# Optimization experiments

Measured on AMD Instinct MI355X. Metric: run time of the kernel, lower is better.

Reference implementation:

```python
import jax, jax.numpy as jnp
import numpy as np

LATENT = 128
K = 1024          # num_embeddings
LENGTH = 128
HID = 200         # LSTM hidden
IN = 768
COND = 1536


def setup_inputs() -> dict:
    key = jax.random.key(0)
    ks = jax.random.split(key, 16)
    B = 256
    x = jax.random.normal(ks[0], (B, 1, LENGTH, IN), dtype=jnp.float32)
    condition = jax.random.normal(ks[1], (B, 1, LENGTH, COND), dtype=jnp.float32)
    noise = jax.random.normal(ks[2], (B, IN), dtype=jnp.float32)
    s = 0.05
    # LSTM params (PyTorch gate order: i, f, g, o)
    W_ih = jax.random.normal(ks[3], (4 * HID, IN), dtype=jnp.float32) * s
    W_hh = jax.random.normal(ks[4], (4 * HID, HID), dtype=jnp.float32) * s
    b_ih = jax.random.normal(ks[5], (4 * HID,), dtype=jnp.float32) * s
    b_hh = jax.random.normal(ks[6], (4 * HID,), dtype=jnp.float32) * s
    # encoder fc: HID -> LATENT
    W_enc = jax.random.normal(ks[7], (LATENT, HID), dtype=jnp.float32) * s
    b_enc = jnp.zeros((LATENT,), dtype=jnp.float32)
    # codebook, uniform(-1/K, 1/K) as in the module
    emb = jax.random.uniform(ks[8], (K, LATENT), minval=-1.0 / K, maxval=1.0 / K, dtype=jnp.float32)
    # decoder MLP
    D1_IN = LATENT + COND + IN  # 2432
    W1 = jax.random.normal(ks[9], (200, D1_IN), dtype=jnp.float32) * s
    b1 = jnp.zeros((200,), dtype=jnp.float32)
    W2 = jax.random.normal(ks[10], (400, 200), dtype=jnp.float32) * s
    b2 = jnp.zeros((400,), dtype=jnp.float32)
    W3 = jax.random.normal(ks[11], (IN, 400), dtype=jnp.float32) * s
    b3 = jnp.zeros((IN,), dtype=jnp.float32)
    return {"x": x, "condition": condition, "noise": noise,
            "W_ih": W_ih, "W_hh": W_hh, "b_ih": b_ih, "b_hh": b_hh,
            "W_enc": W_enc, "b_enc": b_enc, "emb": emb,
            "W1": W1, "b1": b1, "W2": W2, "b2": b2, "W3": W3, "b3": b3}


def _lstm_last_h(xs, W_ih, W_hh, b_ih, b_hh):
    # xs: [B, T, IN] -> final hidden state [B, HID]
    B = xs.shape[0]
    h0 = jnp.zeros((B, HID), dtype=xs.dtype)
    c0 = jnp.zeros((B, HID), dtype=xs.dtype)
    # precompute input projections for all timesteps: [T, B, 4H]
    gates_x = jnp.einsum('bti,gi->tbg', xs, W_ih) + b_ih + b_hh

    def step(carry, gx):
        h, c = carry
        g = gx + h @ W_hh.T  # [B, 4H]
        i, f, gg, o = jnp.split(g, 4, axis=-1)
        c = jax.nn.sigmoid(f) * c + jax.nn.sigmoid(i) * jnp.tanh(gg)
        h = jax.nn.sigmoid(o) * jnp.tanh(c)
        return (h, c), None

    (h, _), _ = jax.lax.scan(step, (h0, c0), gates_x)
    return h


def reference(x, condition, noise, W_ih, W_hh, b_ih, b_hh, W_enc, b_enc, emb,
              W1, b1, W2, b2, W3, b3):
    B = x.shape[0]
    # Encoder
    xs = x.reshape(B, -1, IN)                      # [B, T, 768]
    h = _lstm_last_h(xs, W_ih, W_hh, b_ih, b_hh)   # [B, 200]
    z_e = h @ W_enc.T + b_enc                      # [B, latent]
    # VectorQuantizer: squared-distance argmin + gather
    d = (jnp.sum(z_e * z_e, axis=-1, keepdims=True)
         + jnp.sum(emb * emb, axis=1)
         - 2.0 * z_e @ emb.T)                      # [B, K]
    indices = jnp.argmin(d, axis=-1)               # [B]
    z_q = emb[indices]                             # [B, latent]
    # Decoder (forward uses z_q directly)
    L = LENGTH
    z = jnp.broadcast_to(z_q[:, None, None, :], (B, 1, L, LATENT))
    n = jnp.broadcast_to(noise[:, None, None, :], (B, 1, L, IN))
    zc = jnp.concatenate([z, condition, n], axis=-1)  # [B,1,L,2432]
    h1 = jax.nn.relu(zc @ W1.T + b1)
    h2 = jax.nn.relu(h1 @ W2.T + b2)
    out = jax.nn.sigmoid(h2 @ W3.T + b3)
    return out.reshape(-1, 1, L, IN)
```

## Files before the change

kernel.cpp:

```cpp
#include <hip/hip_runtime.h>
#include <math.h>

typedef unsigned short u16;
typedef u16 u16x8 __attribute__((ext_vector_type(8)));
typedef __bf16 bf16x8 __attribute__((ext_vector_type(8)));
typedef float f32x4 __attribute__((ext_vector_type(4)));

#define HID 200
#define G4H 800
#define TLEN 128
#define LATENT 128
#define NCODES 1024
#define DIN 768
#define DCOND 1536
#define NB 256
#define MROWS (NB * TLEN)
#define LDG 896
#define LDH1 256
#define LDH2 512
#define NOUT 768

#define WSCL 400.0f
#define HSCL 127.0f
#define ISCL (1.0f / (WSCL * HSCL))
#define W4_DWORDS (12 * 800 * 4)
#define W4_BYTES (W4_DWORDS * 4)

__device__ __forceinline__ u16 f2b(float f) {
  union { float f; unsigned u; } v; v.f = f;
  unsigned r = v.u + 0x7fffu + ((v.u >> 16) & 1u);
  return (u16)(r >> 16);
}
__device__ __forceinline__ float b2f(u16 h) {
  union { unsigned u; float f; } v; v.u = ((unsigned)h) << 16;
  return v.f;
}
__device__ __forceinline__ float sigf(float x) { return 1.f / (1.f + __expf(-x)); }
__device__ __forceinline__ float tanh_fast(float x) {
  return 1.f - 2.f / (__expf(2.f * x) + 1.f);
}

__device__ __forceinline__ int dot4(unsigned a, unsigned b, int c) {
#if __has_builtin(__builtin_amdgcn_sdot4)
  return __builtin_amdgcn_sdot4((int)a, (int)b, c, false);
#else
  int s = c;
  s += (int)(signed char)(a) * (int)(signed char)(b);
  s += (int)(signed char)(a >> 8) * (int)(signed char)(b >> 8);
  s += (int)(signed char)(a >> 16) * (int)(signed char)(b >> 16);
  s += (int)(signed char)(a >> 24) * (int)(signed char)(b >> 24);
  return s;
#endif
}

__device__ __forceinline__ void gl16(const void* g, void* l) {
  __builtin_amdgcn_global_load_lds(
      (const __attribute__((address_space(1))) void*)g,
      (__attribute__((address_space(3))) void*)l, 16, 0, 0);
}

__device__ __forceinline__ unsigned cvtpk(float a, float b) {
  unsigned r;
  asm("v_cvt_pk_bf16_f32 %0, %1, %2" : "=v"(r) : "v"(a), "v"(b));
  return r;
}

__global__ void cvt_pad(const float* __restrict__ src, u16* __restrict__ dst,
                        int nr, int nc, int lds, int col0, int NRp, int KP) {
  int i = blockIdx.x * blockDim.x + threadIdx.x;
  if (i >= NRp * KP) return;
  int r = i / KP, c = i - r * KP;
  float v = (r < nr && c < nc) ? src[(size_t)r * lds + col0 + c] : 0.f;
  dst[i] = f2b(v);
}

__global__ void pad_f32(const float* __restrict__ src, float* __restrict__ dst,
                        int n, int npad) {
  int i = blockIdx.x * blockDim.x + threadIdx.x;
  if (i < npad) dst[i] = (i < n) ? src[i] : 0.f;
}

__global__ void pack_whh_i8(const float* __restrict__ Whh, unsigned* __restrict__ W4,
                            unsigned* __restrict__ Wreg,
                            const float* __restrict__ b_ih, const float* __restrict__ b_hh,
                            float* __restrict__ biasc) {
  int i = blockIdx.x * blockDim.x + threadIdx.x;
  if (i < 800 * 50) {
    int row = i / 50, dw = i - row * 50;
    unsigned d = 0;
#pragma unroll
    for (int e = 0; e < 4; ++e) {
      int k = dw * 4 + e;
      float w = Whh[(size_t)row * HID + k] * WSCL;
      int q = (int)lrintf(w);
      q = q > 127 ? 127 : (q < -127 ? -127 : q);
      d |= ((unsigned)(q & 0xFF)) << (8 * e);
    }
    if (dw < 48) {
      W4[(dw >> 2) * 3200 + row * 4 + (dw & 3)] = d;
    } else {
      int r = (row < 400) ? row : row - 400;
      int base = (row < 400) ? 0 : 2;
      Wreg[r * 4 + base + (dw - 48)] = d;
    }
  }
  if (i < LDG) biasc[i] = (i < G4H) ? (b_ih[i] + b_hh[i]) : 0.f;
}

enum { EPI_GATES = 0, EPI_H1 = 1, EPI_H2 = 2, EPI_OUT = 3 };

__device__ __forceinline__ f32x4 mfma16(bf16x8 a, bf16x8 b, f32x4 c) {
  return __builtin_amdgcn_mfma_f32_16x16x32_bf16(a, b, c, 0, 0, 0);
}

template<bool AF32, int EPI>
__global__ __launch_bounds__(256) void gemm_bf16(
    const void* __restrict__ Ap, const u16* __restrict__ Bp,
    void* __restrict__ Cp, int K, int ldc, const float* __restrict__ bias) {
  __shared__ __attribute__((aligned(16))) char AsRaw[AF32 ? 128 * 32 * 4 : 128 * 32 * 2];
  __shared__ __attribute__((aligned(16))) u16 Bs[128 * 32];
  float* Asf = (float*)AsRaw;
  u16* As16 = (u16*)AsRaw;

  const int t = threadIdx.x;
  const int tileN = blockIdx.x * 128;
  const int tileM = blockIdx.y * 128;
  const int l = t & 63;
  const int w = t >> 6;
  const int wr = (w >> 1) * 64;
  const int wc = (w & 1) * 64;
  const int fr = l & 15;
  const int fg = l >> 4;

  const u16* bsrc[2];
  u16* bdst[2];
#pragma unroll
  for (int j = 0; j < 2; ++j) {
    int tb = w * 1024 + j * 4096 + (t & 63) * 16;
    int row = tb >> 6, gd = (tb >> 4) & 3;
    bsrc[j] = Bp + (size_t)(tileN + row) * K + ((gd ^ ((row >> 1) & 3)) << 3);
    bdst[j] = Bs + w * 512 + j * 2048;
  }
  const float* asrcF[4];
  float* adstF[4];
  const u16* asrcH[2];
  u16* adstH[2];
  if constexpr (AF32) {
#pragma unroll
    for (int j = 0; j < 4; ++j) {
      int tb = w * 1024 + j * 4096 + (t & 63) * 16;
      int row = tb >> 7, gd = (tb >> 4) & 7;
      asrcF[j] = (const float*)Ap + (size_t)(tileM + row) * K + ((gd ^ (row & 7)) << 2);
      adstF[j] = Asf + w * 256 + j * 1024;
    }
  } else {
#pragma unroll
    for (int j = 0; j < 2; ++j) {
      int tb = w * 1024 + j * 4096 + (t & 63) * 16;
      int row = tb >> 6, gd = (tb >> 4) & 3;
      asrcH[j] = (const u16*)Ap + (size_t)(tileM + row) * K + ((gd ^ ((row >> 1) & 3)) << 3);
      adstH[j] = As16 + w * 512 + j * 2048;
    }
  }

  f32x4 acc[4][4];
#pragma unroll
  for (int m = 0; m < 4; ++m)
#pragma unroll
    for (int n = 0; n < 4; ++n) {
      f32x4 z = {0.f, 0.f, 0.f, 0.f};
      acc[m][n] = z;
    }

  for (int k0 = 0; k0 < K; k0 += 32) {
#pragma unroll
    for (int j = 0; j < 2; ++j) { gl16(bsrc[j], bdst[j]); bsrc[j] += 32; }
    if constexpr (AF32) {
#pragma unroll
      for (int j = 0; j < 4; ++j) { gl16(asrcF[j], adstF[j]); asrcF[j] += 32; }
    } else {
#pragma unroll
      for (int j = 0; j < 2; ++j) { gl16(asrcH[j], adstH[j]); asrcH[j] += 32; }
    }
    __syncthreads();

    bf16x8 av[4], bv[4];
#pragma unroll
    for (int m = 0; m < 4; ++m) {
      const int row = wr + m * 16 + fr;
      if constexpr (AF32) {
        const int g0 = (2 * fg) ^ (row & 7);
        const int g1 = (2 * fg + 1) ^ (row & 7);
        float4 p0 = *(const float4*)(Asf + row * 32 + g0 * 4);
        float4 p1 = *(const float4*)(Asf + row * 32 + g1 * 4);
        uint4 u;
        u.x = cvtpk(p0.x, p0.y); u.y = cvtpk(p0.z, p0.w);
        u.z = cvtpk(p1.x, p1.y); u.w = cvtpk(p1.z, p1.w);
        av[m] = __builtin_bit_cast(bf16x8, u);
      } else {
        const int g = fg ^ ((row >> 1) & 3);
        av[m] = __builtin_bit_cast(bf16x8, *(const u16x8*)(As16 + row * 32 + g * 8));
      }
    }
#pragma unroll
    for (int n = 0; n < 4; ++n) {
      const int row = wc + n * 16 + fr;
      const int g = fg ^ ((row >> 1) & 3);
      bv[n] = __builtin_bit_cast(bf16x8, *(const u16x8*)(Bs + row * 32 + g * 8));
    }
#pragma unroll
    for (int m = 0; m < 4; ++m)
#pragma unroll
      for (int n = 0; n < 4; ++n)
        acc[m][n] = mfma16(av[m], bv[n], acc[m][n]);
    __syncthreads();
  }

#pragma unroll
  for (int m = 0; m < 4; ++m) {
#pragma unroll
    for (int n = 0; n < 4; ++n) {
      const int gcol = tileN + wc + n * 16 + fr;
      const int growb = tileM + wr + m * 16 + fg * 4;
#pragma unroll
      for (int r = 0; r < 4; ++r) {
        const int grow = growb + r;
        float v = acc[m][n][r];
        if constexpr (EPI == EPI_GATES) {
          v += bias[gcol];
          ((u16*)Cp)[(size_t)grow * ldc + gcol] = f2b(v);
        } else if constexpr (EPI == EPI_H1) {
          v += bias[(grow >> 7) * 256 + gcol];
          v = fmaxf(v, 0.f);
          ((u16*)Cp)[(size_t)grow * ldc + gcol] = f2b(v);
        } else if constexpr (EPI == EPI_H2) {
          v += bias[gcol];
          v = fmaxf(v, 0.f);
          ((u16*)Cp)[(size_t)grow * ldc + gcol] = f2b(v);
        } else {
          v += bias[gcol];
          ((float*)Cp)[(size_t)grow * ldc + gcol] = sigf(v);
        }
      }
    }
  }
}

__global__ __launch_bounds__(448) void lstm_enc(
    const u16* __restrict__ gates, const uint4* __restrict__ W4g,
    const uint4* __restrict__ Wregg,
    const float* __restrict__ Wenc, const float* __restrict__ b_enc,
    const float* __restrict__ emb, const float* __restrict__ W1,
    const float* __restrict__ b1, const float* __restrict__ noise,
    float* __restrict__ p1) {
  extern __shared__ __attribute__((aligned(16))) char dynsm[];
  uint4* W4 = (uint4*)dynsm;
  __shared__ __attribute__((aligned(16))) unsigned sh_hq[56];
  __shared__ __attribute__((aligned(16))) float sh_hf[HID];
  __shared__ float sh_g[G4H];
  __shared__ __attribute__((aligned(16))) float sh_ze[LATENT];
  __shared__ float sh_zq[LATENT];
  __shared__ float sh_rd[448];
  __shared__ int sh_ri[448];
  const int r = threadIdx.x;
  const int b = blockIdx.x;
  const bool active = (r < 400);

  for (int i = r; i < 12 * 800; i += 448) W4[i] = W4g[i];
  uint4 wreg = active ? Wregg[r] : (uint4){0, 0, 0, 0};
  if (r < 56) sh_hq[r] = 0;
  if (r < HID) sh_hf[r] = 0.f;
  float c = 0.f;
  const u16* gp = gates + (size_t)b * TLEN * LDG + r;
  float gvA = 0.f, gvB = 0.f;
  if (active) { gvA = b2f(gp[0]); gvB = b2f(gp[400]); }
  __syncthreads();

  for (int t = 0; t < TLEN; ++t) {
    gp += LDG;
    float gvA_n = 0.f, gvB_n = 0.f;
    if (active && t + 1 < TLEN) { gvA_n = b2f(gp[0]); gvB_n = b2f(gp[400]); }

    if (active) {
      unsigned hd[52];
#pragma unroll
      for (int j = 0; j < 13; ++j) {
        uint4 v = ((const uint4*)sh_hq)[j];
        hd[4 * j + 0] = v.x; hd[4 * j + 1] = v.y;
        hd[4 * j + 2] = v.z; hd[4 * j + 3] = v.w;
      }
      int accA = 0, accB = 0;
#pragma unroll
      for (int jb = 0; jb < 12; ++jb) {
        uint4 wA = W4[jb * 800 + r];
        uint4 wB = W4[jb * 800 + 400 + r];
        accA = dot4(wA.x, hd[4 * jb + 0], accA);
        accA = dot4(wA.y, hd[4 * jb + 1], accA);
        accA = dot4(wA.z, hd[4 * jb + 2], accA);
        accA = dot4(wA.w, hd[4 * jb + 3], accA);
        accB = dot4(wB.x, hd[4 * jb + 0], accB);
        accB = dot4(wB.y, hd[4 * jb + 1], accB);
        accB = dot4(wB.z, hd[4 * jb + 2], accB);
        accB = dot4(wB.w, hd[4 * jb + 3], accB);
      }
      accA = dot4(wreg.x, hd[48], accA);
      accA = dot4(wreg.y, hd[49], accA);
      accB = dot4(wreg.z, hd[48], accB);
      accB = dot4(wreg.w, hd[49], accB);
      sh_g[r] = gvA + (float)accA * ISCL;
      sh_g[r + 400] = gvB + (float)accB * ISCL;
    }
    __syncthreads();
    if (r < HID) {
      float gi = sh_g[r], gf = sh_g[HID + r], gg = sh_g[2 * HID + r], go = sh_g[3 * HID + r];
      c = sigf(gf) * c + sigf(gi) * tanh_fast(gg);
      float h = sigf(go) * tanh_fast(c);
      sh_hf[r] = h;
      int q = __float2int_rn(h * HSCL);
      ((char*)sh_hq)[r] = (char)q;
    }
    __syncthreads();
    gvA = gvA_n; gvB = gvB_n;
  }

  if (r < LATENT) {
    float z = b_enc[r];
#pragma unroll 4
    for (int k = 0; k < HID; ++k) z = fmaf(Wenc[(size_t)r * HID + k], sh_hf[k], z);
    sh_ze[r] = z;
  }
  __syncthreads();

  float best = INFINITY; int bi = 0;
  for (int k = r; k < NCODES; k += 448) {
    float d = 0.f;
#pragma unroll
    for (int q = 0; q < LATENT / 4; ++q) {
      float4 e = *(const float4*)&emb[(size_t)k * LATENT + q * 4];
      float4 z = *(const float4*)&sh_ze[q * 4];
      d += e.x * (e.x - 2.f * z.x) + e.y * (e.y - 2.f * z.y)
         + e.z * (e.z - 2.f * z.z) + e.w * (e.w - 2.f * z.w);
    }
    if (d < best) { best = d; bi = k; }
  }
  sh_rd[r] = best; sh_ri[r] = bi;
  __syncthreads();
  for (int s = 256; s > 0; s >>= 1) {
    if (r < s && r + s < 448) {
      float od = sh_rd[r + s]; int oi = sh_ri[r + s];
      if (od < sh_rd[r] || (od == sh_rd[r] && oi < sh_ri[r])) { sh_rd[r] = od; sh_ri[r] = oi; }
    }
    __syncthreads();
  }
  const int kmin = sh_ri[0];
  if (r < LATENT) sh_zq[r] = emb[(size_t)kmin * LATENT + r];
  __syncthreads();

  if (r < 256) {
    float v = 0.f;
    if (r < HID) {
      v = b1[r];
      const float* wrow = W1 + (size_t)r * 2432;
#pragma unroll 4
      for (int d = 0; d < LATENT; ++d) v = fmaf(wrow[d], sh_zq[d], v);
      const float* nz = noise + (size_t)b * DIN;
#pragma unroll 4
      for (int d = 0; d < DIN; ++d) v = fmaf(wrow[1664 + d], nz[d], v);
    }
    p1[b * 256 + r] = v;
  }
}

extern "C" void kernel_launch(void* const* d_in, const int* in_sizes, int n_in,
                              void* d_out, int out_size, void* d_ws, size_t ws_size,
                              hipStream_t stream) {
  const float* x     = (const float*)d_in[0];
  const float* cond  = (const float*)d_in[1];
  const float* noise = (const float*)d_in[2];
  const float* W_ih  = (const float*)d_in[3];
  const float* W_hh  = (const float*)d_in[4];
  const float* b_ih  = (const float*)d_in[5];
  const float* b_hh  = (const float*)d_in[6];
  const float* W_enc = (const float*)d_in[7];
  const float* b_enc = (const float*)d_in[8];
  const float* emb   = (const float*)d_in[9];
  const float* W1    = (const float*)d_in[10];
  const float* b1    = (const float*)d_in[11];
  const float* W2    = (const float*)d_in[12];
  const float* b2    = (const float*)d_in[13];
  const float* W3    = (const float*)d_in[14];
  const float* b3    = (const float*)d_in[15];

  char* ws = (char*)d_ws;
  size_t off = 0;
  auto alloc = [&](size_t bytes) -> void* {
    void* p = ws + off; off += (bytes + 255) & ~(size_t)255; return p;
  };
  u16*      W_ihb = (u16*)alloc((size_t)896 * 768 * 2);
  u16*      W1cb  = (u16*)alloc((size_t)256 * 1536 * 2);
  u16*      W2b   = (u16*)alloc((size_t)512 * 256 * 2);
  u16*      W3b   = (u16*)alloc((size_t)768 * 512 * 2);
  float*    b2p   = (float*)alloc(512 * 4);
  unsigned* W4    = (unsigned*)alloc((size_t)W4_BYTES);
  unsigned* Wreg  = (unsigned*)alloc((size_t)400 * 4 * 4);
  float*    biasc = (float*)alloc(LDG * 4);
  u16*      gates = (u16*)alloc((size_t)MROWS * LDG * 2);
  float*    p1    = (float*)alloc(256 * 256 * 4);
  u16*      h1    = (u16*)alloc((size_t)MROWS * LDH1 * 2);
  u16*      h2    = (u16*)alloc((size_t)MROWS * LDH2 * 2);

  cvt_pad<<<dim3((896 * 768 + 255) / 256), 256, 0, stream>>>(W_ih, W_ihb, 800, 768, 768, 0, 896, 768);
  cvt_pad<<<dim3((256 * 1536 + 255) / 256), 256, 0, stream>>>(W1, W1cb, 200, 1536, 2432, 128, 256, 1536);
  cvt_pad<<<dim3((512 * 256 + 255) / 256), 256, 0, stream>>>(W2, W2b, 400, 200, 200, 0, 512, 256);
  cvt_pad<<<dim3((768 * 512 + 255) / 256), 256, 0, stream>>>(W3, W3b, 768, 400, 400, 0, 768, 512);
  pad_f32<<<dim3(2), 256, 0, stream>>>(b2, b2p, 400, 512);
  pack_whh_i8<<<dim3((800 * 50 + 255) / 256), 256, 0, stream>>>(W_hh, W4, Wreg, b_ih, b_hh, biasc);

  gemm_bf16<true, EPI_GATES><<<dim3(LDG / 128, MROWS / 128), 256, 0, stream>>>(
      x, W_ihb, gates, 768, LDG, biasc);

  static bool attr_set = false;
  if (!attr_set) {
    (void)hipFuncSetAttribute((const void*)lstm_enc,
                              hipFuncAttributeMaxDynamicSharedMemorySize, W4_BYTES);
    attr_set = true;
  }
  lstm_enc<<<dim3(NB), 448, W4_BYTES, stream>>>(gates, (const uint4*)W4, (const uint4*)Wreg,
                                                W_enc, b_enc, emb, W1, b1, noise, p1);

  gemm_bf16<true, EPI_H1><<<dim3(LDH1 / 128, MROWS / 128), 256, 0, stream>>>(
      cond, W1cb, h1, DCOND, LDH1, p1);
  gemm_bf16<false, EPI_H2><<<dim3(LDH2 / 128, MROWS / 128), 256, 0, stream>>>(
      h1, W2b, h2, LDH1, LDH2, b2p);
  gemm_bf16<false, EPI_OUT><<<dim3(NOUT / 128, MROWS / 128), 256, 0, stream>>>(
      h2, W3b, (float*)d_out, LDH2, NOUT, b3);
}
```

Before: 552.6 us.

## Compute all four LSTM gates per hidden unit in-thread, double-buffer h

The LSTM step is restructured so each of 200 threads computes all four gate dot products for one hidden unit and applies the cell update directly. This removes the shared-memory gate exchange and halves the barriers per timestep by double-buffering the quantized hidden state. The block shrinks from 448 to 256 threads, and the tail-weight layout is repacked to match. Each thread now does twice the dot-product work per step with fewer threads in flight, so per-step latency could grow.

```diff
diff --git a/kernel.cpp b/kernel.cpp
--- a/kernel.cpp
+++ b/kernel.cpp
@@ -23,8 +23,8 @@
 #define WSCL 400.0f
 #define HSCL 127.0f
 #define ISCL (1.0f / (WSCL * HSCL))
-#define W4_DWORDS (12 * 800 * 4)
-#define W4_BYTES (W4_DWORDS * 4)
+#define W4_UINT4 (12 * 800)
+#define W4_BYTES (W4_UINT4 * 16)
 
 __device__ __forceinline__ u16 f2b(float f) {
   union { float f; unsigned u; } v; v.f = f;
@@ -97,11 +97,10 @@
       d |= ((unsigned)(q & 0xFF)) << (8 * e);
     }
     if (dw < 48) {
-      W4[(dw >> 2) * 3200 + row * 4 + (dw & 3)] = d;
+      W4[((dw >> 2) * 800 + row) * 4 + (dw & 3)] = d;
     } else {
-      int r = (row < 400) ? row : row - 400;
-      int base = (row < 400) ? 0 : 2;
-      Wreg[r * 4 + base + (dw - 48)] = d;
+      int g = row / 200, u = row - g * 200;
+      Wreg[u * 8 + g * 2 + (dw - 48)] = d;
     }
   }
   if (i < LDG) biasc[i] = (i < G4H) ? (b_ih[i] + b_hh[i]) : 0.f;
@@ -246,82 +245,89 @@
   }
 }
 
-__global__ __launch_bounds__(448) void lstm_enc(
+__global__ __launch_bounds__(256) void lstm_enc(
     const u16* __restrict__ gates, const uint4* __restrict__ W4g,
-    const uint4* __restrict__ Wregg,
+    const uint4* __restrict__ WregG,
     const float* __restrict__ Wenc, const float* __restrict__ b_enc,
     const float* __restrict__ emb, const float* __restrict__ W1,
     const float* __restrict__ b1, const float* __restrict__ noise,
     float* __restrict__ p1) {
   extern __shared__ __attribute__((aligned(16))) char dynsm[];
   uint4* W4 = (uint4*)dynsm;
-  __shared__ __attribute__((aligned(16))) unsigned sh_hq[56];
+  __shared__ __attribute__((aligned(16))) unsigned sh_hq[2][56];
   __shared__ __attribute__((aligned(16))) float sh_hf[HID];
-  __shared__ float sh_g[G4H];
   __shared__ __attribute__((aligned(16))) float sh_ze[LATENT];
   __shared__ float sh_zq[LATENT];
-  __shared__ float sh_rd[448];
-  __shared__ int sh_ri[448];
+  __shared__ float sh_rd[256];
+  __shared__ int sh_ri[256];
   const int r = threadIdx.x;
   const int b = blockIdx.x;
-  const bool active = (r < 400);
-
-  for (int i = r; i < 12 * 800; i += 448) W4[i] = W4g[i];
-  uint4 wreg = active ? Wregg[r] : (uint4){0, 0, 0, 0};
-  if (r < 56) sh_hq[r] = 0;
-  if (r < HID) sh_hf[r] = 0.f;
-  float c = 0.f;
+  const bool worker = (r < 200);
+
+  for (int i = r; i < W4_UINT4; i += 256) W4[i] = W4g[i];
+  uint4 wt0 = {0, 0, 0, 0}, wt1 = {0, 0, 0, 0};
+  if (worker) { wt0 = WregG[r * 2]; wt1 = WregG[r * 2 + 1]; }
+  if (r < 56) { sh_hq[0][r] = 0; sh_hq[1][r] = 0; }
+  float c = 0.f, hlast = 0.f;
   const u16* gp = gates + (size_t)b * TLEN * LDG + r;
-  float gvA = 0.f, gvB = 0.f;
-  if (active) { gvA = b2f(gp[0]); gvB = b2f(gp[400]); }
+  float gv0 = 0.f, gv1 = 0.f, gv2 = 0.f, gv3 = 0.f;
+  if (worker) {
+    gv0 = b2f(gp[0]); gv1 = b2f(gp[200]);
+    gv2 = b2f(gp[400]); gv3 = b2f(gp[600]);
+  }
   __syncthreads();
 
   for (int t = 0; t < TLEN; ++t) {
     gp += LDG;
-    float gvA_n = 0.f, gvB_n = 0.f;
-    if (active && t + 1 < TLEN) { gvA_n = b2f(gp[0]); gvB_n = b2f(gp[400]); }
-
-    if (active) {
+    float gn0 = 0.f, gn1 = 0.f, gn2 = 0.f, gn3 = 0.f;
+    if (worker && t + 1 < TLEN) {
+      gn0 = b2f(gp[0]); gn1 = b2f(gp[200]);
+      gn2 = b2f(gp[400]); gn3 = b2f(gp[600]);
+    }
+    const int cur = t & 1, nxt = cur ^ 1;
+
+    if (worker) {
       unsigned hd[52];
 #pragma unroll
       for (int j = 0; j < 13; ++j) {
-        uint4 v = ((const uint4*)sh_hq)[j];
+        uint4 v = ((const uint4*)sh_hq[cur])[j];
         hd[4 * j + 0] = v.x; hd[4 * j + 1] = v.y;
         hd[4 * j + 2] = v.z; hd[4 * j + 3] = v.w;
       }
-      int accA = 0, accB = 0;
+      int a0 = 0, a1 = 0, a2 = 0, a3 = 0;
 #pragma unroll
       for (int jb = 0; jb < 12; ++jb) {
-        uint4 wA = W4[jb * 800 + r];
-        uint4 wB = W4[jb * 800 + 400 + r];
-        accA = dot4(wA.x, hd[4 * jb + 0], accA);
-        accA = dot4(wA.y, hd[4 * jb + 1], accA);
-        accA = dot4(wA.z, hd[4 * jb + 2], accA);
-        accA = dot4(wA.w, hd[4 * jb + 3], accA);
-        accB = dot4(wB.x, hd[4 * jb + 0], accB);
-        accB = dot4(wB.y, hd[4 * jb + 1], accB);
-        accB = dot4(wB.z, hd[4 * jb + 2], accB);
-        accB = dot4(wB.w, hd[4 * jb + 3], accB);
+        uint4 w0 = W4[jb * 800 + r];
+        uint4 w1 = W4[jb * 800 + 200 + r];
+        uint4 w2 = W4[jb * 800 + 400 + r];
+        uint4 w3 = W4[jb * 800 + 600 + r];
+#pragma unroll
+        for (int e = 0; e < 4; ++e) {
+          unsigned h = hd[jb * 4 + e];
+          a0 = dot4((&w0.x)[e], h, a0);
+          a1 = dot4((&w1.x)[e], h, a1);
+          a2 = dot4((&w2.x)[e], h, a2);
+          a3 = dot4((&w3.x)[e], h, a3);
+        }
       }
-      accA = dot4(wreg.x, hd[48], accA);
-      accA = dot4(wreg.y, hd[49], accA);
-      accB = dot4(wreg.z, hd[48], accB);
-      accB = dot4(wreg.w, hd[49], accB);
-      sh_g[r] = gvA + (float)accA * ISCL;
-      sh_g[r + 400] = gvB + (float)accB * ISCL;
+      a0 = dot4(wt0.x, hd[48], a0); a0 = dot4(wt0.y, hd[49], a0);
+      a1 = dot4(wt0.z, hd[48], a1); a1 = dot4(wt0.w, hd[49], a1);
+      a2 = dot4(wt1.x, hd[48], a2); a2 = dot4(wt1.y, hd[49], a2);
+      a3 = dot4(wt1.z, hd[48], a3); a3 = dot4(wt1.w, hd[49], a3);
+      float gi = gv0 + (float)a0 * ISCL;
+      float gf = gv1 + (float)a1 * ISCL;
+      float gg = gv2 + (float)a2 * ISCL;
+      float go = gv3 + (float)a3 * ISCL;
+      c = sigf(gf) * c + sigf(gi) * tanh_fast(gg);
+      hlast = sigf(go) * tanh_fast(c);
+      ((char*)sh_hq[nxt])[r] = (char)__float2int_rn(hlast * HSCL);
     }
     __syncthreads();
-    if (r < HID) {
-      float gi = sh_g[r], gf = sh_g[HID + r], gg = sh_g[2 * HID + r], go = sh_g[3 * HID + r];
-      c = sigf(gf) * c + sigf(gi) * tanh_fast(gg);
-      float h = sigf(go) * tanh_fast(c);
-      sh_hf[r] = h;
-      int q = __float2int_rn(h * HSCL);
-      ((char*)sh_hq)[r] = (char)q;
-    }
-    __syncthreads();
-    gvA = gvA_n; gvB = gvB_n;
-  }
+    gv0 = gn0; gv1 = gn1; gv2 = gn2; gv3 = gn3;
+  }
+
+  if (worker) sh_hf[r] = hlast;
+  __syncthreads();
 
   if (r < LATENT) {
     float z = b_enc[r];
@@ -332,7 +338,7 @@
   __syncthreads();
 
   float best = INFINITY; int bi = 0;
-  for (int k = r; k < NCODES; k += 448) {
+  for (int k = r; k < NCODES; k += 256) {
     float d = 0.f;
 #pragma unroll
     for (int q = 0; q < LATENT / 4; ++q) {
@@ -345,8 +351,8 @@
   }
   sh_rd[r] = best; sh_ri[r] = bi;
   __syncthreads();
-  for (int s = 256; s > 0; s >>= 1) {
-    if (r < s && r + s < 448) {
+  for (int s = 128; s > 0; s >>= 1) {
+    if (r < s) {
       float od = sh_rd[r + s]; int oi = sh_ri[r + s];
       if (od < sh_rd[r] || (od == sh_rd[r] && oi < sh_ri[r])) { sh_rd[r] = od; sh_ri[r] = oi; }
     }
@@ -356,9 +362,9 @@
   if (r < LATENT) sh_zq[r] = emb[(size_t)kmin * LATENT + r];
   __syncthreads();
 
-  if (r < 256) {
+  {
     float v = 0.f;
-    if (r < HID) {
+    if (worker) {
       v = b1[r];
       const float* wrow = W1 + (size_t)r * 2432;
 #pragma unroll 4
@@ -402,7 +408,7 @@
   u16*      W3b   = (u16*)alloc((size_t)768 * 512 * 2);
   float*    b2p   = (float*)alloc(512 * 4);
   unsigned* W4    = (unsigned*)alloc((size_t)W4_BYTES);
-  unsigned* Wreg  = (unsigned*)alloc((size_t)400 * 4 * 4);
+  unsigned* Wreg  = (unsigned*)alloc((size_t)200 * 8 * 4);
   float*    biasc = (float*)alloc(LDG * 4);
   u16*      gates = (u16*)alloc((size_t)MROWS * LDG * 2);
   float*    p1    = (float*)alloc(256 * 256 * 4);
@@ -425,7 +431,7 @@
                               hipFuncAttributeMaxDynamicSharedMemorySize, W4_BYTES);
     attr_set = true;
   }
-  lstm_enc<<<dim3(NB), 448, W4_BYTES, stream>>>(gates, (const uint4*)W4, (const uint4*)Wreg,
+  lstm_enc<<<dim3(NB), 256, W4_BYTES, stream>>>(gates, (const uint4*)W4, (const uint4*)Wreg,
                                                 W_enc, b_enc, emb, W1, b1, noise, p1);
 
   gemm_bf16<true, EPI_H1><<<dim3(LDH1 / 128, MROWS / 128), 256, 0, stream>>>(
```

After: 555.4 us. About the same (+0.5%).
